# Optimization experiments

Measured on AMD Instinct MI355X. Metric: run time of the kernel, lower is better.

Reference implementation:

```python
import jax, jax.numpy as jnp
import numpy as np

N, E = 20000, 320000
IN_DIM = OUT_DIM = E_IN = E_OUT = 128
BN_EPS = 1e-5

def _lrelu(x):
    return jnp.where(x >= 0, x, 0.1 * x)

def setup_inputs() -> dict:
    key = jax.random.key(0)
    ks = jax.random.split(key, 12)
    def w(k, shape):
        return jax.random.normal(k, shape, jnp.float32) * (shape[0] ** -0.5)
    return {
        "h": jax.random.normal(ks[0], (N, IN_DIM), jnp.float32),
        "edge_w": jax.random.normal(ks[1], (E, E_IN), jnp.float32),
        "W_node": w(ks[2], (IN_DIM, OUT_DIM)),
        "W_eedge": w(ks[3], (E_IN, E_IN)),
        "W_esf": w(ks[4], (E_IN, 1)),
        "W_fuse": w(ks[5], (2 * OUT_DIM + E_IN, OUT_DIM)),
        "b_fuse": jnp.zeros((OUT_DIM,), jnp.float32),
        "W_attn": w(ks[6], (OUT_DIM, 1)),
        "W_conc": w(ks[7], (2 * OUT_DIM + E_IN, OUT_DIM)),
        "b_conc": jnp.zeros((OUT_DIM,), jnp.float32),
        "bn_gamma": jnp.ones((E_IN,), jnp.float32),
        "bn_beta": jnp.zeros((E_IN,), jnp.float32),
        "W_aggre": w(ks[8], (2 * OUT_DIM + 2 * E_IN, E_OUT)),
        "src": jax.random.randint(ks[9], (E,), 0, N),
        "dst": jax.random.randint(ks[10], (E,), 0, N),
    }

def reference(h, edge_w, W_node, W_eedge, W_esf, W_fuse, b_fuse, W_attn,
              W_conc, b_conc, bn_gamma, bn_beta, W_aggre, src, dst):
    # eval mode: dropout = identity, BatchNorm uses running stats (mean 0, var 1)
    hn = h @ W_node                       # embed_node -> ndata['h'] = ndata['oh']
    # self_attention: ow = embed_edge(w); w = edge_sf_atten(lrelu(ow)) * ow
    ow = edge_w @ W_eedge                 # [E, e_in]
    w1 = (_lrelu(ow) @ W_esf) * ow        # [E, e_in]
    # inter_attention
    hs, hd = hn[src], hn[dst]             # [E, out]
    sat = jnp.concatenate([hs, hd, w1], axis=-1)          # [E, 2*out+e_in]
    inw = _lrelu(sat @ W_fuse + b_fuse)                   # [E, out]
    a = inw @ W_attn                                      # [E, 1]
    w2 = a * w1                                           # edata['w']
    # reduce_func2: segment softmax over incoming edges (grouped by dst)
    s = a[:, 0]
    m = jax.ops.segment_max(s, dst, num_segments=N)
    e = jnp.exp(s - m[dst])
    denom = jax.ops.segment_sum(e, dst, num_segments=N)
    alpha = (e / denom[dst])[:, None]                     # [E, 1]
    t = jnp.concatenate([hs, w2], axis=-1)                # [E, out+e_in]
    h_agg = jax.ops.segment_sum(alpha * t, dst, num_segments=N)  # [N, out+e_in]
    h_new = jnp.concatenate([h_agg, hn], axis=-1) @ W_conc + b_conc
    # DGL only updates nodes that received messages; zero-indegree keep embed_node(h)
    indeg = jax.ops.segment_sum(jnp.ones((E,), jnp.float32), dst, num_segments=N)
    h_out = jnp.where(indeg[:, None] > 0, h_new, hn)      # [N, out]
    # edge_calc: BN(w2) then aggre_embed_edge(cat(src_h, dst_h, bn_w, ow))
    w_bn = (w2 / jnp.sqrt(jnp.float32(1.0) + BN_EPS)) * bn_gamma + bn_beta
    z = jnp.concatenate([h_out[src], h_out[dst], w_bn, ow], axis=-1)
    w_out = z @ W_aggre                                   # [E, e_out]
    return h_out, w_out, sat
```

## Files before the change

### kernel.cpp

```cpp
#include <hip/hip_runtime.h>
#include <hip/hip_bf16.h>

#define TB 256
#define BM 64
#define BK 32
#define BN 128
#define ASTR 68
#define MAXD 160

static constexpr int NN = 20000;
static constexpr int NE = 320000;

static constexpr long long OFF_HN   = 0;
static constexpr long long OFF_OW   = 2560000;
static constexpr long long OFF_S    = 43520000;
static constexpr long long OFF_DEN  = 43840000;
static constexpr long long OFF_CUR  = 43860000;
static constexpr long long OFF_HAGG = 43880000;
static constexpr long long OFF_WT   = 49000000;
static constexpr long long WS_FLOATS = 49140000;

static constexpr int U_E = 0;
static constexpr int U_F = 32768;
static constexpr int U_A = 131072;

static constexpr long long OUT_HOUT = 0;
static constexpr long long OUT_WOUT = 2560000;
static constexpr long long OUT_SAT  = 43520000;

typedef __attribute__((ext_vector_type(8))) short s8v;
typedef __attribute__((ext_vector_type(4))) float f32x4;

#define MFMA16(a,b,c) __builtin_amdgcn_mfma_f32_16x16x32_bf16(a,b,c,0,0,0)

__device__ __forceinline__ float lrelu(float x){ return x >= 0.f ? x : 0.1f*x; }

__device__ __forceinline__ void split1(float f, unsigned short& hi, unsigned short& lo){
    __hip_bfloat16 h = __float2bfloat16(f);
    float hf = __bfloat162float(h);
    __hip_bfloat16 l = __float2bfloat16(f - hf);
    hi = __builtin_bit_cast(unsigned short, h);
    lo = __builtin_bit_cast(unsigned short, l);
}
__device__ __forceinline__ void split8(float4 a, float4 b, s8v& hi, s8v& lo){
    float v[8] = {a.x,a.y,a.z,a.w,b.x,b.y,b.z,b.w};
#pragma unroll
    for (int j = 0; j < 8; ++j){
        unsigned short hs, ls;
        split1(v[j], hs, ls);
        hi[j] = (short)hs; lo[j] = (short)ls;
    }
}

__device__ __forceinline__ int lds_a(int row, int g){
    return row*32 + ((g ^ (row & 3)) << 3);
}

__device__ __forceinline__ void store_At(float (*Ast)[ASTR], int k4, int r, float4 v){
    Ast[k4+0][r] = v.x; Ast[k4+1][r] = v.y; Ast[k4+2][r] = v.z; Ast[k4+3][r] = v.w;
}
__device__ __forceinline__ void mm_chunk(const float (*Ast)[ASTR], const float (*Bs)[BN],
                                         int r0, int c0, float acc[4][8]){
#pragma unroll 4
    for (int k = 0; k < BK; ++k){
        const float4 av = *(const float4*)&Ast[k][r0];
        const float4 b0 = *(const float4*)&Bs[k][c0];
        const float4 b1 = *(const float4*)&Bs[k][64 + c0];
        const float a0=av.x, a1=av.y, a2=av.z, a3=av.w;
        const float b[8] = {b0.x,b0.y,b0.z,b0.w,b1.x,b1.y,b1.z,b1.w};
#pragma unroll
        for (int j = 0; j < 8; ++j){
            acc[0][j] = fmaf(a0, b[j], acc[0][j]);
            acc[1][j] = fmaf(a1, b[j], acc[1][j]);
            acc[2][j] = fmaf(a2, b[j], acc[2][j]);
            acc[3][j] = fmaf(a3, b[j], acc[3][j]);
        }
    }
}
__device__ __forceinline__ void load_B(const float* __restrict__ W, int kc,
                                       float (*Bs)[BN], int tid){
#pragma unroll
    for (int p = 0; p < 4; ++p){
        int idx = p*TB + tid;
        int row = idx >> 5;
        int c4  = (idx & 31) << 2;
        *(float4*)&Bs[row][c4] = *(const float4*)&W[(size_t)(kc+row)*BN + c4];
    }
}

__device__ __forceinline__ float blockMax(float v, float* sh4){
#pragma unroll
    for (int m = 32; m; m >>= 1) v = fmaxf(v, __shfl_xor(v, m));
    if ((threadIdx.x & 63) == 0) sh4[threadIdx.x >> 6] = v;
    __syncthreads();
    float r = fmaxf(fmaxf(sh4[0], sh4[1]), fmaxf(sh4[2], sh4[3]));
    __syncthreads();
    return r;
}
__device__ __forceinline__ float blockSum(float v, float* sh4){
#pragma unroll
    for (int m = 32; m; m >>= 1) v += __shfl_xor(v, m);
    if ((threadIdx.x & 63) == 0) sh4[threadIdx.x >> 6] = v;
    __syncthreads();
    float r = sh4[0] + sh4[1] + sh4[2] + sh4[3];
    __syncthreads();
    return r;
}

__global__ __launch_bounds__(TB) void kA_init(int* __restrict__ cur){
    int i = blockIdx.x*TB + threadIdx.x;
    if (i < NN) cur[i] = 0;
}
__global__ __launch_bounds__(TB) void kB_count(const int* __restrict__ dst,
                                               int* __restrict__ cur){
    int e = blockIdx.x*TB + threadIdx.x;
    atomicAdd(&cur[dst[e]], 1);
}
__global__ __launch_bounds__(TB) void kC_scan(int* __restrict__ cur,
                                              int* __restrict__ offs){
    __shared__ int part[TB];
    __shared__ int spre[TB];
    const int tid = threadIdx.x;
    const int CH = (NN + TB - 1) / TB;
    const int base = tid * CH;
    int sum = 0;
    for (int i = 0; i < CH; ++i){ int idx = base + i; if (idx < NN) sum += cur[idx]; }
    part[tid] = sum;
    __syncthreads();
    if (tid == 0){ int r = 0; for (int i = 0; i < TB; ++i){ spre[i] = r; r += part[i]; } }
    __syncthreads();
    int run = spre[tid];
    for (int i = 0; i < CH; ++i){
        int idx = base + i;
        if (idx < NN){ int c = cur[idx]; offs[idx] = run; cur[idx] = run; run += c; }
    }
}
__global__ __launch_bounds__(TB) void kD_scatter(const int* __restrict__ dst,
                                                 int* __restrict__ cur,
                                                 int* __restrict__ eidx){
    int e = blockIdx.x*TB + threadIdx.x;
    int p = atomicAdd(&cur[dst[e]], 1);
    eidx[p] = e;
}

__global__ __launch_bounds__(TB) void kW_prep(const float* __restrict__ W,
                                              unsigned short* __restrict__ wtH,
                                              unsigned short* __restrict__ wtL,
                                              int K){
    int id = blockIdx.x*TB + threadIdx.x;
    if (id >= 128*K) return;
    int n = id / K, k = id - n*K;
    unsigned short hs, ls;
    split1(W[(size_t)k*128 + n], hs, ls);
    wtH[id] = hs; wtL[id] = ls;
}

__global__ __launch_bounds__(TB) void k1_hn(const float* __restrict__ h,
                                            const float* __restrict__ Wn,
                                            float* __restrict__ hn){
    __shared__ float Ast[BK][ASTR];
    __shared__ float Bs[BK][BN];
    const int tid = threadIdx.x;
    const int rbase = blockIdx.x * BM;
    const int tc = tid & 15, tr = tid >> 4;
    const int r0 = tr*4, c0 = tc*4;
    float acc[4][8] = {};
    for (int kc = 0; kc < 128; kc += BK){
        __syncthreads();
        {
            int lr = tid >> 3, k4 = (tid & 7) << 2;
#pragma unroll
            for (int p = 0; p < 2; ++p){
                int r = p*32 + lr;
                int rr = rbase + r; if (rr >= NN) rr = NN-1;
                float4 v = *(const float4*)&h[(size_t)rr*128 + kc + k4];
                store_At(Ast, k4, r, v);
            }
        }
        load_B(Wn, kc, Bs, tid);
        __syncthreads();
        mm_chunk(Ast, Bs, r0, c0, acc);
    }
#pragma unroll
    for (int i = 0; i < 4; ++i){
        int rr = rbase + r0 + i;
        if (rr < NN){
            float4 o0 = {acc[i][0],acc[i][1],acc[i][2],acc[i][3]};
            float4 o1 = {acc[i][4],acc[i][5],acc[i][6],acc[i][7]};
            *(float4*)&hn[(size_t)rr*128 + c0] = o0;
            *(float4*)&hn[(size_t)rr*128 + 64 + c0] = o1;
        }
    }
}


__global__ __launch_bounds__(TB) void k2_mfma(const float* __restrict__ ew,
                                              const unsigned short* __restrict__ wtH,
                                              const unsigned short* __restrict__ wtL,
                                              const float* __restrict__ Wesf,
                                              float* __restrict__ ow,
                                              float* __restrict__ sat){
    __shared__ __align__(16) unsigned short Ah[4096], Al[4096], Bh[4096], Bl[4096];
    __shared__ float sEsf[128];
    const int tid = threadIdx.x;
    const long long rbase = (long long)blockIdx.x * 128;
    const int lane = tid & 63, w = tid >> 6;
    const int ls = lane & 15, lg = lane >> 4;
    if (tid < 128) sEsf[tid] = Wesf[tid];
    f32x4 acc[2][8] = {};
    for (int kc = 0; kc < 128; kc += 32){
        __syncthreads();
#pragma unroll
        for (int u = 0; u < 2; ++u){
            int id = tid + u*256;
            int row = id >> 2, g = id & 3;
            int kk = kc + g*8;
            const float* p = &ew[(rbase + row)*128 + kk];
            float4 v0 = *(const float4*)p, v1 = *(const float4*)(p+4);
            s8v hi, lo; split8(v0, v1, hi, lo);
            *(s8v*)&Ah[lds_a(row,g)] = hi; *(s8v*)&Al[lds_a(row,g)] = lo;
            int col = row;
            *(s8v*)&Bh[lds_a(col,g)] = *(const s8v*)&wtH[col*128 + kk];
            *(s8v*)&Bl[lds_a(col,g)] = *(const s8v*)&wtL[col*128 + kk];
        }
        __syncthreads();
        s8v ah[2], al[2];
#pragma unroll
        for (int rt = 0; rt < 2; ++rt){
            int r = w*32 + rt*16 + ls;
            ah[rt] = *(const s8v*)&Ah[lds_a(r,lg)];
            al[rt] = *(const s8v*)&Al[lds_a(r,lg)];
        }
#pragma unroll
        for (int ct = 0; ct < 8; ++ct){
            int c = ct*16 + ls;
            s8v bh = *(const s8v*)&Bh[lds_a(c,lg)];
            s8v bl = *(const s8v*)&Bl[lds_a(c,lg)];
#pragma unroll
            for (int rt = 0; rt < 2; ++rt){
                acc[rt][ct] = MFMA16(ah[rt], bh, acc[rt][ct]);
                acc[rt][ct] = MFMA16(ah[rt], bl, acc[rt][ct]);
                acc[rt][ct] = MFMA16(al[rt], bh, acc[rt][ct]);
            }
        }
    }
#pragma unroll
    for (int rt = 0; rt < 2; ++rt){
#pragma unroll
        for (int reg = 0; reg < 4; ++reg){
            float p = 0.f;
#pragma unroll
            for (int ct = 0; ct < 8; ++ct)
                p += lrelu(acc[rt][ct][reg]) * sEsf[ct*16 + ls];
#pragma unroll
            for (int m = 1; m < 16; m <<= 1) p += __shfl_xor(p, m);
            long long orow = rbase + w*32 + rt*16 + lg*4 + reg;
#pragma unroll
            for (int ct = 0; ct < 8; ++ct){
                float o = acc[rt][ct][reg];
                int col = ct*16 + ls;
                ow[orow*128 + col] = o;
                sat[orow*384 + 256 + col] = p * o;
            }
        }
    }
}

__global__ __launch_bounds__(TB) void k3_mfma(const float* __restrict__ hn,
                                              const unsigned short* __restrict__ wtH,
                                              const unsigned short* __restrict__ wtL,
                                              const float* __restrict__ bf,
                                              const float* __restrict__ Wattn,
                                              const int* __restrict__ src,
                                              const int* __restrict__ dst,
                                              float* __restrict__ sat,
                                              float* __restrict__ w2,
                                              float* __restrict__ s_ws){
    __shared__ __align__(16) unsigned short Ah[4096], Al[4096], Bh[4096], Bl[4096];
    __shared__ float sBf[128], sAtt[128];
    __shared__ int sSrc[128], sDst[128];
    const int tid = threadIdx.x;
    const long long rbase = (long long)blockIdx.x * 128;
    const int lane = tid & 63, w = tid >> 6;
    const int ls = lane & 15, lg = lane >> 4;
    if (tid < 128){
        sBf[tid] = bf[tid]; sAtt[tid] = Wattn[tid];
        sSrc[tid] = src[rbase + tid]; sDst[tid] = dst[rbase + tid];
    }
    f32x4 acc[2][8] = {};
    for (int kc = 0; kc < 384; kc += 32){
        __syncthreads();
#pragma unroll
        for (int u = 0; u < 2; ++u){
            int id = tid + u*256;
            int row = id >> 2, g = id & 3;
            int kk = kc + g*8;
            long long e = rbase + row;
            float4 v0, v1;
            if (kk < 128){
                const float* p = &hn[(size_t)sSrc[row]*128 + kk];
                v0 = *(const float4*)p; v1 = *(const float4*)(p+4);
                *(float4*)&sat[e*384 + kk] = v0; *(float4*)&sat[e*384 + kk + 4] = v1;
            } else if (kk < 256){
                const float* p = &hn[(size_t)sDst[row]*128 + (kk-128)];
                v0 = *(const float4*)p; v1 = *(const float4*)(p+4);
                *(float4*)&sat[e*384 + kk] = v0; *(float4*)&sat[e*384 + kk + 4] = v1;
            } else {
                const float* p = &sat[e*384 + kk];
                v0 = *(const float4*)p; v1 = *(const float4*)(p+4);
            }
            s8v hi, lo; split8(v0, v1, hi, lo);
            *(s8v*)&Ah[lds_a(row,g)] = hi; *(s8v*)&Al[lds_a(row,g)] = lo;
            int col = row;
            *(s8v*)&Bh[lds_a(col,g)] = *(const s8v*)&wtH[col*384 + kk];
            *(s8v*)&Bl[lds_a(col,g)] = *(const s8v*)&wtL[col*384 + kk];
        }
        __syncthreads();
        s8v ah[2], al[2];
#pragma unroll
        for (int rt = 0; rt < 2; ++rt){
            int r = w*32 + rt*16 + ls;
            ah[rt] = *(const s8v*)&Ah[lds_a(r,lg)];
            al[rt] = *(const s8v*)&Al[lds_a(r,lg)];
        }
#pragma unroll
        for (int ct = 0; ct < 8; ++ct){
            int c = ct*16 + ls;
            s8v bh = *(const s8v*)&Bh[lds_a(c,lg)];
            s8v bl = *(const s8v*)&Bl[lds_a(c,lg)];
#pragma unroll
            for (int rt = 0; rt < 2; ++rt){
                acc[rt][ct] = MFMA16(ah[rt], bh, acc[rt][ct]);
                acc[rt][ct] = MFMA16(ah[rt], bl, acc[rt][ct]);
                acc[rt][ct] = MFMA16(al[rt], bh, acc[rt][ct]);
            }
        }
    }
#pragma unroll
    for (int rt = 0; rt < 2; ++rt){
#pragma unroll
        for (int reg = 0; reg < 4; ++reg){
            float p = 0.f;
#pragma unroll
            for (int ct = 0; ct < 8; ++ct){
                int col = ct*16 + ls;
                p += lrelu(acc[rt][ct][reg] + sBf[col]) * sAtt[col];
            }
#pragma unroll
            for (int m = 1; m < 16; m <<= 1) p += __shfl_xor(p, m);
            long long orow = rbase + w*32 + rt*16 + lg*4 + reg;
            if (ls == 0) s_ws[orow] = p;
#pragma unroll
            for (int ct = 0; ct < 8; ++ct){
                int col = ct*16 + ls;
                float w1 = sat[orow*384 + 256 + col];
                w2[orow*128 + col] = p * w1;
            }
        }
    }
}

__global__ __launch_bounds__(TB) void k5_agg(const float* __restrict__ s,
                                             const float* __restrict__ hn,
                                             const float* __restrict__ w2,
                                             const int* __restrict__ src,
                                             const int* __restrict__ eidx,
                                             const int* __restrict__ offs,
                                             const int* __restrict__ cur,
                                             float* __restrict__ hagg,
                                             float* __restrict__ den){
    __shared__ int   sE[MAXD];
    __shared__ int   sSrc[MAXD];
    __shared__ float sA[MAXD];
    __shared__ float sh4[4];
    const int n = blockIdx.x, tid = threadIdx.x;
    const int start = offs[n];
    const int deg = cur[n] - start;
    for (int i = tid; i < deg && i < MAXD; i += TB) sE[i] = eidx[start+i];
    __syncthreads();
    if (tid == 0 && deg > 1){
        int dd = deg < MAXD ? deg : MAXD;
        for (int i = 1; i < dd; ++i){
            int key = sE[i], j = i-1;
            while (j >= 0 && sE[j] > key){ sE[j+1] = sE[j]; --j; }
            sE[j+1] = key;
        }
    }
    __syncthreads();
    float lm = -3.402823466e38f;
    for (int i = tid; i < deg; i += TB){
        int e = (i < MAXD) ? sE[i] : eidx[start+i];
        lm = fmaxf(lm, s[e]);
    }
    const float m = blockMax(lm, sh4);
    float lsum = 0.f;
    for (int i = tid; i < deg; i += TB){
        int e = (i < MAXD) ? sE[i] : eidx[start+i];
        lsum += expf(s[e] - m);
    }
    const float denom = blockSum(lsum, sh4);
    for (int i = tid; i < deg && i < MAXD; i += TB){
        int e = sE[i];
        sA[i] = expf(s[e] - m) / denom;
        sSrc[i] = src[e];
    }
    __syncthreads();
    float acc = 0.f;
    const bool lo = tid < 128;
    for (int i = 0; i < deg; ++i){
        int e, sI; float a;
        if (i < MAXD){ e = sE[i]; a = sA[i]; sI = sSrc[i]; }
        else { e = eidx[start+i]; a = expf(s[e]-m)/denom; sI = src[e]; }
        float v = lo ? hn[(size_t)sI*128 + tid] : w2[(size_t)e*128 + (tid-128)];
        acc = fmaf(a, v, acc);
    }
    hagg[(size_t)n*256 + tid] = acc;
    if (tid == 0) den[n] = (deg > 0) ? denom : 0.f;
}

__global__ __launch_bounds__(TB) void k6_conc(const float* __restrict__ hagg,
                                              const float* __restrict__ hn,
                                              const float* __restrict__ Wc,
                                              const float* __restrict__ bc,
                                              const float* __restrict__ den,
                                              float* __restrict__ hout){
    __shared__ float Ast[BK][ASTR];
    __shared__ float Bs[BK][BN];
    __shared__ float sBc[BN];
    const int tid = threadIdx.x;
    const int rbase = blockIdx.x * BM;
    const int tc = tid & 15, tr = tid >> 4;
    const int r0 = tr*4, c0 = tc*4;
    if (tid < BN) sBc[tid] = bc[tid];
    float acc[4][8] = {};
    for (int chunk = 0; chunk < 12; ++chunk){
        int kc = chunk * BK;
        __syncthreads();
        {
            int lr = tid >> 3, k4 = (tid & 7) << 2;
#pragma unroll
            for (int p = 0; p < 2; ++p){
                int r = p*32 + lr;
                int rr = rbase + r; if (rr >= NN) rr = NN-1;
                float4 v;
                if (chunk < 8) v = *(const float4*)&hagg[(size_t)rr*256 + kc + k4];
                else           v = *(const float4*)&hn[(size_t)rr*128 + (kc-256) + k4];
                store_At(Ast, k4, r, v);
            }
        }
        load_B(Wc, kc, Bs, tid);
        __syncthreads();
        mm_chunk(Ast, Bs, r0, c0, acc);
    }
#pragma unroll
    for (int i = 0; i < 4; ++i){
        int rr = rbase + r0 + i;
        if (rr >= NN) continue;
        bool keep = den[rr] > 0.f;
        float4 h0 = *(const float4*)&hn[(size_t)rr*128 + c0];
        float4 h1 = *(const float4*)&hn[(size_t)rr*128 + 64 + c0];
        float4 o0, o1;
        o0.x = keep ? acc[i][0] + sBc[c0+0] : h0.x;
        o0.y = keep ? acc[i][1] + sBc[c0+1] : h0.y;
        o0.z = keep ? acc[i][2] + sBc[c0+2] : h0.z;
        o0.w = keep ? acc[i][3] + sBc[c0+3] : h0.w;
        o1.x = keep ? acc[i][4] + sBc[64+c0+0] : h1.x;
        o1.y = keep ? acc[i][5] + sBc[64+c0+1] : h1.y;
        o1.z = keep ? acc[i][6] + sBc[64+c0+2] : h1.z;
        o1.w = keep ? acc[i][7] + sBc[64+c0+3] : h1.w;
        *(float4*)&hout[(size_t)rr*128 + c0] = o0;
        *(float4*)&hout[(size_t)rr*128 + 64 + c0] = o1;
    }
}

__global__ __launch_bounds__(TB) void k7_mfma(const float* __restrict__ hout,
                                              const float* __restrict__ ow,
                                              const float* __restrict__ gamma,
                                              const float* __restrict__ beta,
                                              const unsigned short* __restrict__ wtH,
                                              const unsigned short* __restrict__ wtL,
                                              const int* __restrict__ src,
                                              const int* __restrict__ dst,
                                              float* __restrict__ w2out){
    __shared__ __align__(16) unsigned short Ah[4096], Al[4096], Bh[4096], Bl[4096];
    __shared__ float sGam[128], sBet[128];
    __shared__ int sSrc[128], sDst[128];
    const int tid = threadIdx.x;
    const long long rbase = (long long)blockIdx.x * 128;
    const int lane = tid & 63, w = tid >> 6;
    const int ls = lane & 15, lg = lane >> 4;
    const float ISR = 0.9999950000374997f;
    if (tid < 128){
        sGam[tid] = gamma[tid] * ISR; sBet[tid] = beta[tid];
        sSrc[tid] = src[rbase + tid]; sDst[tid] = dst[rbase + tid];
    }
    f32x4 acc[2][8] = {};
    for (int kc = 0; kc < 512; kc += 32){
        __syncthreads();
#pragma unroll
        for (int u = 0; u < 2; ++u){
            int id = tid + u*256;
            int row = id >> 2, g = id & 3;
            int kk = kc + g*8;
            long long e = rbase + row;
            float4 v0, v1;
            if (kk < 128){
                const float* p = &hout[(size_t)sSrc[row]*128 + kk];
                v0 = *(const float4*)p; v1 = *(const float4*)(p+4);
            } else if (kk < 256){
                const float* p = &hout[(size_t)sDst[row]*128 + (kk-128)];
                v0 = *(const float4*)p; v1 = *(const float4*)(p+4);
            } else if (kk < 384){
                int cb = kk - 256;
                const float* p = &w2out[e*128 + cb];
                v0 = *(const float4*)p; v1 = *(const float4*)(p+4);
                v0.x = fmaf(v0.x, sGam[cb+0], sBet[cb+0]);
                v0.y = fmaf(v0.y, sGam[cb+1], sBet[cb+1]);
                v0.z = fmaf(v0.z, sGam[cb+2], sBet[cb+2]);
                v0.w = fmaf(v0.w, sGam[cb+3], sBet[cb+3]);
                v1.x = fmaf(v1.x, sGam[cb+4], sBet[cb+4]);
                v1.y = fmaf(v1.y, sGam[cb+5], sBet[cb+5]);
                v1.z = fmaf(v1.z, sGam[cb+6], sBet[cb+6]);
                v1.w = fmaf(v1.w, sGam[cb+7], sBet[cb+7]);
            } else {
                const float* p = &ow[e*128 + (kk-384)];
                v0 = *(const float4*)p; v1 = *(const float4*)(p+4);
            }
            s8v hi, lo; split8(v0, v1, hi, lo);
            *(s8v*)&Ah[lds_a(row,g)] = hi; *(s8v*)&Al[lds_a(row,g)] = lo;
            int col = row;
            *(s8v*)&Bh[lds_a(col,g)] = *(const s8v*)&wtH[col*512 + kk];
            *(s8v*)&Bl[lds_a(col,g)] = *(const s8v*)&wtL[col*512 + kk];
        }
        __syncthreads();
        s8v ah[2], al[2];
#pragma unroll
        for (int rt = 0; rt < 2; ++rt){
            int r = w*32 + rt*16 + ls;
            ah[rt] = *(const s8v*)&Ah[lds_a(r,lg)];
            al[rt] = *(const s8v*)&Al[lds_a(r,lg)];
        }
#pragma unroll
        for (int ct = 0; ct < 8; ++ct){
            int c = ct*16 + ls;
            s8v bh = *(const s8v*)&Bh[lds_a(c,lg)];
            s8v bl = *(const s8v*)&Bl[lds_a(c,lg)];
#pragma unroll
            for (int rt = 0; rt < 2; ++rt){
                acc[rt][ct] = MFMA16(ah[rt], bh, acc[rt][ct]);
                acc[rt][ct] = MFMA16(ah[rt], bl, acc[rt][ct]);
                acc[rt][ct] = MFMA16(al[rt], bh, acc[rt][ct]);
            }
        }
    }
#pragma unroll
    for (int rt = 0; rt < 2; ++rt){
#pragma unroll
        for (int reg = 0; reg < 4; ++reg){
            long long orow = rbase + w*32 + rt*16 + lg*4 + reg;
#pragma unroll
            for (int ct = 0; ct < 8; ++ct)
                w2out[orow*128 + ct*16 + ls] = acc[rt][ct][reg];
        }
    }
}

extern "C" void kernel_launch(void* const* d_in, const int* in_sizes, int n_in,
                              void* d_out, int out_size, void* d_ws, size_t ws_size,
                              hipStream_t stream){
    (void)in_sizes; (void)n_in; (void)out_size;
    const float* h       = (const float*)d_in[0];
    const float* edge_w  = (const float*)d_in[1];
    const float* W_node  = (const float*)d_in[2];
    const float* W_eedge = (const float*)d_in[3];
    const float* W_esf   = (const float*)d_in[4];
    const float* W_fuse  = (const float*)d_in[5];
    const float* b_fuse  = (const float*)d_in[6];
    const float* W_attn  = (const float*)d_in[7];
    const float* W_conc  = (const float*)d_in[8];
    const float* b_conc  = (const float*)d_in[9];
    const float* gamma   = (const float*)d_in[10];
    const float* beta    = (const float*)d_in[11];
    const float* W_aggre = (const float*)d_in[12];
    const int*   src     = (const int*)d_in[13];
    const int*   dst     = (const int*)d_in[14];

    float* out    = (float*)d_out;
    float* o_hout = out + OUT_HOUT;
    float* o_wout = out + OUT_WOUT;
    float* o_sat  = out + OUT_SAT;

    if (ws_size < (size_t)WS_FLOATS * 4) return;
    float* ws     = (float*)d_ws;
    float* w_hn   = ws + OFF_HN;
    float* w_ow   = ws + OFF_OW;
    float* w_s    = ws + OFF_S;
    float* w_den  = ws + OFF_DEN;
    int*   w_cur  = (int*)(ws + OFF_CUR);
    float* w_hagg = ws + OFF_HAGG;
    unsigned short* w_wt = (unsigned short*)(ws + OFF_WT);

    int* w_eidx = (int*)o_hout;
    int* w_offs = w_eidx + NE;

    hipLaunchKernelGGL(kA_init,   dim3((NN+TB-1)/TB), dim3(TB), 0, stream, w_cur);
    hipLaunchKernelGGL(kB_count,  dim3(NE/TB), dim3(TB), 0, stream, dst, w_cur);
    hipLaunchKernelGGL(kC_scan,   dim3(1), dim3(TB), 0, stream, w_cur, w_offs);
    hipLaunchKernelGGL(kD_scatter,dim3(NE/TB), dim3(TB), 0, stream, dst, w_cur, w_eidx);

    hipLaunchKernelGGL(kW_prep, dim3((128*128+TB-1)/TB), dim3(TB), 0, stream,
                       W_eedge, w_wt + U_E, w_wt + U_E + 128*128, 128);
    hipLaunchKernelGGL(kW_prep, dim3((128*384+TB-1)/TB), dim3(TB), 0, stream,
                       W_fuse,  w_wt + U_F, w_wt + U_F + 128*384, 384);
    hipLaunchKernelGGL(kW_prep, dim3((128*512+TB-1)/TB), dim3(TB), 0, stream,
                       W_aggre, w_wt + U_A, w_wt + U_A + 128*512, 512);

    hipLaunchKernelGGL(k1_hn,   dim3((NN+BM-1)/BM), dim3(TB), 0, stream, h, W_node, w_hn);
    hipLaunchKernelGGL(k2_mfma, dim3(NE/128), dim3(TB), 0, stream, edge_w,
                       w_wt + U_E, w_wt + U_E + 128*128, W_esf, w_ow, o_sat);
    hipLaunchKernelGGL(k3_mfma, dim3(NE/128), dim3(TB), 0, stream, w_hn,
                       w_wt + U_F, w_wt + U_F + 128*384, b_fuse, W_attn,
                       src, dst, o_sat, o_wout, w_s);
    hipLaunchKernelGGL(k5_agg,  dim3(NN), dim3(TB), 0, stream, w_s, w_hn, o_wout,
                       src, w_eidx, w_offs, w_cur, w_hagg, w_den);
    hipLaunchKernelGGL(k6_conc, dim3((NN+BM-1)/BM), dim3(TB), 0, stream, w_hagg, w_hn,
                       W_conc, b_conc, w_den, o_hout);
    hipLaunchKernelGGL(k7_mfma, dim3(NE/128), dim3(TB), 0, stream, o_hout, w_ow,
                       gamma, beta, w_wt + U_A, w_wt + U_A + 128*512,
                       src, dst, o_wout);
}
```

Baseline: 850.6 us.

## Fuse edge-embed and fuse GEMMs, store ow as bf16 split, merge prep kernels

Merges the edge-embedding GEMM kernel and the fuse/attention GEMM kernel into one kernel per 128-edge tile, so the tile's w1 stays cache-hot between the two phases and one launch is removed. The intermediate ow is now stored as pre-split bf16 hi/lo halves instead of fp32, so the final GEMM loads them straight into shared memory without re-splitting. The three weight-prep launches and the counter init are merged into a single prep kernel. In exchange the fused kernel carries more shared memory and register state, which may lower occupancy.

```diff
diff --git a/kernel.cpp b/kernel.cpp
--- a/kernel.cpp
+++ b/kernel.cpp
@@ -107,10 +107,31 @@
     return r;
 }
 
-__global__ __launch_bounds__(TB) void kA_init(int* __restrict__ cur){
-    int i = blockIdx.x*TB + threadIdx.x;
-    if (i < NN) cur[i] = 0;
-}
+__global__ __launch_bounds__(TB) void k_prep(const float* __restrict__ We,
+                                             const float* __restrict__ Wf,
+                                             const float* __restrict__ Wa,
+                                             unsigned short* __restrict__ wt,
+                                             int* __restrict__ cur){
+    int id = blockIdx.x*TB + threadIdx.x;
+    if (id < NN) cur[id] = 0;
+    unsigned short hs, ls;
+    if (id < 16384){
+        int n = id >> 7, k = id & 127;
+        split1(We[(size_t)k*128 + n], hs, ls);
+        wt[U_E + id] = hs; wt[U_E + 16384 + id] = ls;
+    } else if (id < 65536){
+        int local = id - 16384;
+        int n = local / 384, k = local - n*384;
+        split1(Wf[(size_t)k*128 + n], hs, ls);
+        wt[U_F + local] = hs; wt[U_F + 49152 + local] = ls;
+    } else if (id < 131072){
+        int local = id - 65536;
+        int n = local >> 9, k = local & 511;
+        split1(Wa[(size_t)k*128 + n], hs, ls);
+        wt[U_A + local] = hs; wt[U_A + 65536 + local] = ls;
+    }
+}
+
 __global__ __launch_bounds__(TB) void kB_count(const int* __restrict__ dst,
                                                int* __restrict__ cur){
     int e = blockIdx.x*TB + threadIdx.x;
@@ -141,18 +162,6 @@
     int e = blockIdx.x*TB + threadIdx.x;
     int p = atomicAdd(&cur[dst[e]], 1);
     eidx[p] = e;
-}
-
-__global__ __launch_bounds__(TB) void kW_prep(const float* __restrict__ W,
-                                              unsigned short* __restrict__ wtH,
-                                              unsigned short* __restrict__ wtL,
-                                              int K){
-    int id = blockIdx.x*TB + threadIdx.x;
-    if (id >= 128*K) return;
-    int n = id / K, k = id - n*K;
-    unsigned short hs, ls;
-    split1(W[(size_t)k*128 + n], hs, ls);
-    wtH[id] = hs; wtL[id] = ls;
 }
 
 __global__ __launch_bounds__(TB) void k1_hn(const float* __restrict__ h,
@@ -193,20 +202,33 @@
     }
 }
 
-
-__global__ __launch_bounds__(TB) void k2_mfma(const float* __restrict__ ew,
-                                              const unsigned short* __restrict__ wtH,
-                                              const unsigned short* __restrict__ wtL,
-                                              const float* __restrict__ Wesf,
-                                              float* __restrict__ ow,
-                                              float* __restrict__ sat){
+__global__ __launch_bounds__(TB) void k23_fuse(const float* __restrict__ ew,
+                                               const unsigned short* __restrict__ wtE_H,
+                                               const unsigned short* __restrict__ wtE_L,
+                                               const float* __restrict__ Wesf,
+                                               const unsigned short* __restrict__ wtF_H,
+                                               const unsigned short* __restrict__ wtF_L,
+                                               const float* __restrict__ bf,
+                                               const float* __restrict__ Wattn,
+                                               const int* __restrict__ src,
+                                               const int* __restrict__ dst,
+                                               const float* __restrict__ hn,
+                                               unsigned short* __restrict__ owH,
+                                               unsigned short* __restrict__ owL,
+                                               float* __restrict__ sat,
+                                               float* __restrict__ w2,
+                                               float* __restrict__ s_ws){
     __shared__ __align__(16) unsigned short Ah[4096], Al[4096], Bh[4096], Bl[4096];
-    __shared__ float sEsf[128];
+    __shared__ float sEsf[128], sBf[128], sAtt[128];
+    __shared__ int sSrc[128], sDst[128];
     const int tid = threadIdx.x;
     const long long rbase = (long long)blockIdx.x * 128;
     const int lane = tid & 63, w = tid >> 6;
     const int ls = lane & 15, lg = lane >> 4;
-    if (tid < 128) sEsf[tid] = Wesf[tid];
+    if (tid < 128){
+        sEsf[tid] = Wesf[tid]; sBf[tid] = bf[tid]; sAtt[tid] = Wattn[tid];
+        sSrc[tid] = src[rbase + tid]; sDst[tid] = dst[rbase + tid];
+    }
     f32x4 acc[2][8] = {};
     for (int kc = 0; kc < 128; kc += 32){
         __syncthreads();
@@ -220,8 +242,8 @@
             s8v hi, lo; split8(v0, v1, hi, lo);
             *(s8v*)&Ah[lds_a(row,g)] = hi; *(s8v*)&Al[lds_a(row,g)] = lo;
             int col = row;
-            *(s8v*)&Bh[lds_a(col,g)] = *(const s8v*)&wtH[col*128 + kk];
-            *(s8v*)&Bl[lds_a(col,g)] = *(const s8v*)&wtL[col*128 + kk];
+            *(s8v*)&Bh[lds_a(col,g)] = *(const s8v*)&wtE_H[col*128 + kk];
+            *(s8v*)&Bl[lds_a(col,g)] = *(const s8v*)&wtE_L[col*128 + kk];
         }
         __syncthreads();
         s8v ah[2], al[2];
@@ -259,35 +281,19 @@
             for (int ct = 0; ct < 8; ++ct){
                 float o = acc[rt][ct][reg];
                 int col = ct*16 + ls;
-                ow[orow*128 + col] = o;
                 sat[orow*384 + 256 + col] = p * o;
-            }
-        }
-    }
-}
-
-__global__ __launch_bounds__(TB) void k3_mfma(const float* __restrict__ hn,
-                                              const unsigned short* __restrict__ wtH,
-                                              const unsigned short* __restrict__ wtL,
-                                              const float* __restrict__ bf,
-                                              const float* __restrict__ Wattn,
-                                              const int* __restrict__ src,
-                                              const int* __restrict__ dst,
-                                              float* __restrict__ sat,
-                                              float* __restrict__ w2,
-                                              float* __restrict__ s_ws){
-    __shared__ __align__(16) unsigned short Ah[4096], Al[4096], Bh[4096], Bl[4096];
-    __shared__ float sBf[128], sAtt[128];
-    __shared__ int sSrc[128], sDst[128];
-    const int tid = threadIdx.x;
-    const long long rbase = (long long)blockIdx.x * 128;
-    const int lane = tid & 63, w = tid >> 6;
-    const int ls = lane & 15, lg = lane >> 4;
-    if (tid < 128){
-        sBf[tid] = bf[tid]; sAtt[tid] = Wattn[tid];
-        sSrc[tid] = src[rbase + tid]; sDst[tid] = dst[rbase + tid];
-    }
-    f32x4 acc[2][8] = {};
+                unsigned short hsv, lsv; split1(o, hsv, lsv);
+                owH[orow*128 + col] = hsv;
+                owL[orow*128 + col] = lsv;
+            }
+        }
+    }
+    __threadfence_block();
+#pragma unroll
+    for (int rt = 0; rt < 2; ++rt)
+#pragma unroll
+        for (int ct = 0; ct < 8; ++ct)
+            acc[rt][ct] = (f32x4){0.f, 0.f, 0.f, 0.f};
     for (int kc = 0; kc < 384; kc += 32){
         __syncthreads();
 #pragma unroll
@@ -312,8 +318,8 @@
             s8v hi, lo; split8(v0, v1, hi, lo);
             *(s8v*)&Ah[lds_a(row,g)] = hi; *(s8v*)&Al[lds_a(row,g)] = lo;
             int col = row;
-            *(s8v*)&Bh[lds_a(col,g)] = *(const s8v*)&wtH[col*384 + kk];
-            *(s8v*)&Bl[lds_a(col,g)] = *(const s8v*)&wtL[col*384 + kk];
+            *(s8v*)&Bh[lds_a(col,g)] = *(const s8v*)&wtF_H[col*384 + kk];
+            *(s8v*)&Bl[lds_a(col,g)] = *(const s8v*)&wtF_L[col*384 + kk];
         }
         __syncthreads();
         s8v ah[2], al[2];
@@ -353,8 +359,8 @@
 #pragma unroll
             for (int ct = 0; ct < 8; ++ct){
                 int col = ct*16 + ls;
-                float w1 = sat[orow*384 + 256 + col];
-                w2[orow*128 + col] = p * w1;
+                float w1v = sat[orow*384 + 256 + col];
+                w2[orow*128 + col] = p * w1v;
             }
         }
     }
@@ -474,7 +480,8 @@
 }
 
 __global__ __launch_bounds__(TB) void k7_mfma(const float* __restrict__ hout,
-                                              const float* __restrict__ ow,
+                                              const unsigned short* __restrict__ owH,
+                                              const unsigned short* __restrict__ owL,
                                               const float* __restrict__ gamma,
                                               const float* __restrict__ beta,
                                               const unsigned short* __restrict__ wtH,
@@ -503,31 +510,33 @@
             int row = id >> 2, g = id & 3;
             int kk = kc + g*8;
             long long e = rbase + row;
-            float4 v0, v1;
-            if (kk < 128){
-                const float* p = &hout[(size_t)sSrc[row]*128 + kk];
-                v0 = *(const float4*)p; v1 = *(const float4*)(p+4);
-            } else if (kk < 256){
-                const float* p = &hout[(size_t)sDst[row]*128 + (kk-128)];
-                v0 = *(const float4*)p; v1 = *(const float4*)(p+4);
-            } else if (kk < 384){
-                int cb = kk - 256;
-                const float* p = &w2out[e*128 + cb];
-                v0 = *(const float4*)p; v1 = *(const float4*)(p+4);
-                v0.x = fmaf(v0.x, sGam[cb+0], sBet[cb+0]);
-                v0.y = fmaf(v0.y, sGam[cb+1], sBet[cb+1]);
-                v0.z = fmaf(v0.z, sGam[cb+2], sBet[cb+2]);
-                v0.w = fmaf(v0.w, sGam[cb+3], sBet[cb+3]);
-                v1.x = fmaf(v1.x, sGam[cb+4], sBet[cb+4]);
-                v1.y = fmaf(v1.y, sGam[cb+5], sBet[cb+5]);
-                v1.z = fmaf(v1.z, sGam[cb+6], sBet[cb+6]);
-                v1.w = fmaf(v1.w, sGam[cb+7], sBet[cb+7]);
+            if (kk < 384){
+                float4 v0, v1;
+                if (kk < 128){
+                    const float* p = &hout[(size_t)sSrc[row]*128 + kk];
+                    v0 = *(const float4*)p; v1 = *(const float4*)(p+4);
+                } else if (kk < 256){
+                    const float* p = &hout[(size_t)sDst[row]*128 + (kk-128)];
+                    v0 = *(const float4*)p; v1 = *(const float4*)(p+4);
+                } else {
+                    int cb = kk - 256;
+                    const float* p = &w2out[e*128 + cb];
+                    v0 = *(const float4*)p; v1 = *(const float4*)(p+4);
+                    v0.x = fmaf(v0.x, sGam[cb+0], sBet[cb+0]);
+                    v0.y = fmaf(v0.y, sGam[cb+1], sBet[cb+1]);
+                    v0.z = fmaf(v0.z, sGam[cb+2], sBet[cb+2]);
+                    v0.w = fmaf(v0.w, sGam[cb+3], sBet[cb+3]);
+                    v1.x = fmaf(v1.x, sGam[cb+4], sBet[cb+4]);
+                    v1.y = fmaf(v1.y, sGam[cb+5], sBet[cb+5]);
+                    v1.z = fmaf(v1.z, sGam[cb+6], sBet[cb+6]);
+                    v1.w = fmaf(v1.w, sGam[cb+7], sBet[cb+7]);
+                }
+                s8v hi, lo; split8(v0, v1, hi, lo);
+                *(s8v*)&Ah[lds_a(row,g)] = hi; *(s8v*)&Al[lds_a(row,g)] = lo;
             } else {
-                const float* p = &ow[e*128 + (kk-384)];
-                v0 = *(const float4*)p; v1 = *(const float4*)(p+4);
-            }
-            s8v hi, lo; split8(v0, v1, hi, lo);
-            *(s8v*)&Ah[lds_a(row,g)] = hi; *(s8v*)&Al[lds_a(row,g)] = lo;
+                *(s8v*)&Ah[lds_a(row,g)] = *(const s8v*)&owH[e*128 + (kk-384)];
+                *(s8v*)&Al[lds_a(row,g)] = *(const s8v*)&owL[e*128 + (kk-384)];
+            }
             int col = row;
             *(s8v*)&Bh[lds_a(col,g)] = *(const s8v*)&wtH[col*512 + kk];
             *(s8v*)&Bl[lds_a(col,g)] = *(const s8v*)&wtL[col*512 + kk];
@@ -593,7 +602,8 @@
     if (ws_size < (size_t)WS_FLOATS * 4) return;
     float* ws     = (float*)d_ws;
     float* w_hn   = ws + OFF_HN;
-    float* w_ow   = ws + OFF_OW;
+    unsigned short* w_owH = (unsigned short*)(ws + OFF_OW);
+    unsigned short* w_owL = w_owH + (size_t)NE*128;
     float* w_s    = ws + OFF_S;
     float* w_den  = ws + OFF_DEN;
     int*   w_cur  = (int*)(ws + OFF_CUR);
@@ -603,29 +613,22 @@
     int* w_eidx = (int*)o_hout;
     int* w_offs = w_eidx + NE;
 
-    hipLaunchKernelGGL(kA_init,   dim3((NN+TB-1)/TB), dim3(TB), 0, stream, w_cur);
+    hipLaunchKernelGGL(k_prep,    dim3(131072/TB), dim3(TB), 0, stream,
+                       W_eedge, W_fuse, W_aggre, w_wt, w_cur);
     hipLaunchKernelGGL(kB_count,  dim3(NE/TB), dim3(TB), 0, stream, dst, w_cur);
     hipLaunchKernelGGL(kC_scan,   dim3(1), dim3(TB), 0, stream, w_cur, w_offs);
     hipLaunchKernelGGL(kD_scatter,dim3(NE/TB), dim3(TB), 0, stream, dst, w_cur, w_eidx);
-
-    hipLaunchKernelGGL(kW_prep, dim3((128*128+TB-1)/TB), dim3(TB), 0, stream,
-                       W_eedge, w_wt + U_E, w_wt + U_E + 128*128, 128);
-    hipLaunchKernelGGL(kW_prep, dim3((128*384+TB-1)/TB), dim3(TB), 0, stream,
-                       W_fuse,  w_wt + U_F, w_wt + U_F + 128*384, 384);
-    hipLaunchKernelGGL(kW_prep, dim3((128*512+TB-1)/TB), dim3(TB), 0, stream,
-                       W_aggre, w_wt + U_A, w_wt + U_A + 128*512, 512);
-
-    hipLaunchKernelGGL(k1_hn,   dim3((NN+BM-1)/BM), dim3(TB), 0, stream, h, W_node, w_hn);
-    hipLaunchKernelGGL(k2_mfma, dim3(NE/128), dim3(TB), 0, stream, edge_w,
-                       w_wt + U_E, w_wt + U_E + 128*128, W_esf, w_ow, o_sat);
-    hipLaunchKernelGGL(k3_mfma, dim3(NE/128), dim3(TB), 0, stream, w_hn,
+    hipLaunchKernelGGL(k1_hn,     dim3((NN+BM-1)/BM), dim3(TB), 0, stream, h, W_node, w_hn);
+    hipLaunchKernelGGL(k23_fuse,  dim3(NE/128), dim3(TB), 0, stream, edge_w,
+                       w_wt + U_E, w_wt + U_E + 128*128, W_esf,
                        w_wt + U_F, w_wt + U_F + 128*384, b_fuse, W_attn,
-                       src, dst, o_sat, o_wout, w_s);
-    hipLaunchKernelGGL(k5_agg,  dim3(NN), dim3(TB), 0, stream, w_s, w_hn, o_wout,
+                       src, dst, w_hn, w_owH, w_owL, o_sat, o_wout, w_s);
+    hipLaunchKernelGGL(k5_agg,    dim3(NN), dim3(TB), 0, stream, w_s, w_hn, o_wout,
                        src, w_eidx, w_offs, w_cur, w_hagg, w_den);
-    hipLaunchKernelGGL(k6_conc, dim3((NN+BM-1)/BM), dim3(TB), 0, stream, w_hagg, w_hn,
+    hipLaunchKernelGGL(k6_conc,   dim3((NN+BM-1)/BM), dim3(TB), 0, stream, w_hagg, w_hn,
                        W_conc, b_conc, w_den, o_hout);
-    hipLaunchKernelGGL(k7_mfma, dim3(NE/128), dim3(TB), 0, stream, o_hout, w_ow,
-                       gamma, beta, w_wt + U_A, w_wt + U_A + 128*512,
+    hipLaunchKernelGGL(k7_mfma,   dim3(NE/128), dim3(TB), 0, stream, o_hout,
+                       w_owH, w_owL, gamma, beta,
+                       w_wt + U_A, w_wt + U_A + 128*512,
                        src, dst, o_wout);
 }
```

Result: slower. 910.1 us (+7.0%).
